# Optimization experiments

Hardware: AMD Instinct MI355X
Metric: run time of the kernel (lower is better)

Reference implementation:

```python
import jax, jax.numpy as jnp
import numpy as np

D_MODEL = 1024
DIM_FF = 4096
N_EXPERTS = 8
TOPK = 2
N_TOKENS = 8192


def setup_inputs() -> dict:
    key = jax.random.key(0)
    ks = jax.random.split(key, 8)
    s_in = 1.0 / np.sqrt(D_MODEL)
    s_ff = 1.0 / np.sqrt(DIM_FF)
    x = jax.random.normal(ks[0], (N_TOKENS, D_MODEL), dtype=jnp.float32)
    Wg = jax.random.uniform(ks[1], (D_MODEL, N_EXPERTS), minval=-s_in, maxval=s_in, dtype=jnp.float32)
    bg = jax.random.uniform(ks[2], (N_EXPERTS,), minval=-s_in, maxval=s_in, dtype=jnp.float32)
    W1 = jax.random.uniform(ks[3], (N_EXPERTS, D_MODEL, DIM_FF), minval=-s_in, maxval=s_in, dtype=jnp.float32)
    b1 = jax.random.uniform(ks[4], (N_EXPERTS, DIM_FF), minval=-s_in, maxval=s_in, dtype=jnp.float32)
    W2 = jax.random.uniform(ks[5], (N_EXPERTS, DIM_FF, D_MODEL), minval=-s_ff, maxval=s_ff, dtype=jnp.float32)
    b2 = jax.random.uniform(ks[6], (N_EXPERTS, D_MODEL), minval=-s_ff, maxval=s_ff, dtype=jnp.float32)
    return {"x": x, "Wg": Wg, "bg": bg, "W1": W1, "b1": b1, "W2": W2, "b2": b2}


def reference(x, Wg, bg, W1, b1, W2, b2):
    # Gate: softmax over experts
    w = jax.nn.softmax(x @ Wg + bg, axis=-1)  # [N, E]
    # Sparse gating: keep top-k, renormalize (matches torch scatter mask)
    _, idx = jax.lax.top_k(w, TOPK)  # [N, K]
    n = w.shape[0]
    mask = jnp.zeros_like(w).at[jnp.arange(n)[:, None], idx].set(1.0)
    w = w * mask
    w = w / (jnp.sum(w, axis=-1, keepdims=True) + 1e-9)
    # Dense per-expert FFN (exact GELU, as torch nn.GELU default)
    h = jax.nn.gelu(jnp.einsum('nd,edf->enf', x, W1) + b1[:, None, :], approximate=False)  # [E,N,F]
    y = jnp.einsum('enf,efd->end', h, W2) + b2[:, None, :]  # [E,N,D]
    out = jnp.einsum('ne,end->nd', w, y)  # weighted combine
    return out
```

## Files before the change

### kernel.cpp

```cpp
#include <hip/hip_runtime.h>
#include <cstdint>

typedef unsigned short u16;
typedef unsigned int u32;

#define N_TOKENS 8192
#define D_MODEL 1024
#define DIM_FF 4096
#define N_EXPERTS 8
#define MAX_SLOTS (N_TOKENS * 2)

typedef __bf16 bf16x8 __attribute__((ext_vector_type(8)));
typedef float f32x4 __attribute__((ext_vector_type(4)));

__device__ __forceinline__ u16 f2bf(float f) {
  u32 u = __float_as_uint(f);
  u32 r = (u + 0x7FFFu + ((u >> 16) & 1u)) >> 16;
  return (u16)r;
}
__device__ __forceinline__ u16 bfc(float f) {
  __bf16 b = (__bf16)f;
  return __builtin_bit_cast(u16, b);
}

__device__ __forceinline__ void gl2lds16(const void* g, void* l) {
  __builtin_amdgcn_global_load_lds(
      (__attribute__((address_space(1))) void*)(g),
      (__attribute__((address_space(3))) void*)(l), 16, 0, 0);
}

__global__ __launch_bounds__(256) void gate_kernel(
    const float* __restrict__ x, const float* __restrict__ Wg,
    const float* __restrict__ bg, int* __restrict__ eidx,
    float* __restrict__ ew, u16* __restrict__ xb) {
  int tok = (int)((blockIdx.x * 256 + threadIdx.x) >> 6);
  int lane = threadIdx.x & 63;
  const float* xr = x + (size_t)tok * D_MODEL;
  u16* xbr = xb + (size_t)tok * D_MODEL;
  float acc[8] = {0.f, 0.f, 0.f, 0.f, 0.f, 0.f, 0.f, 0.f};
#pragma unroll
  for (int j = 0; j < 8; ++j) {
    int d = 2 * lane + 128 * j;
    float2 xv = *(const float2*)(xr + d);
    float4 wa0 = *(const float4*)(Wg + d * 8);
    float4 wb0 = *(const float4*)(Wg + d * 8 + 4);
    float4 wa1 = *(const float4*)(Wg + d * 8 + 8);
    float4 wb1 = *(const float4*)(Wg + d * 8 + 12);
    acc[0] += xv.x * wa0.x + xv.y * wa1.x;
    acc[1] += xv.x * wa0.y + xv.y * wa1.y;
    acc[2] += xv.x * wa0.z + xv.y * wa1.z;
    acc[3] += xv.x * wa0.w + xv.y * wa1.w;
    acc[4] += xv.x * wb0.x + xv.y * wb1.x;
    acc[5] += xv.x * wb0.y + xv.y * wb1.y;
    acc[6] += xv.x * wb0.z + xv.y * wb1.z;
    acc[7] += xv.x * wb0.w + xv.y * wb1.w;
    u32 pk = (u32)f2bf(xv.x) | ((u32)f2bf(xv.y) << 16);
    *(u32*)(xbr + d) = pk;
  }
#pragma unroll
  for (int off = 32; off > 0; off >>= 1) {
#pragma unroll
    for (int e = 0; e < 8; ++e) acc[e] += __shfl_xor(acc[e], off, 64);
  }
  if (lane == 0) {
    float p[8], m = -1e30f;
#pragma unroll
    for (int e = 0; e < 8; ++e) { p[e] = acc[e] + bg[e]; m = fmaxf(m, p[e]); }
    float s = 0.f;
#pragma unroll
    for (int e = 0; e < 8; ++e) { p[e] = __expf(p[e] - m); s += p[e]; }
#pragma unroll
    for (int e = 0; e < 8; ++e) p[e] /= s;
    int i0 = 0;
#pragma unroll
    for (int e = 1; e < 8; ++e) if (p[e] > p[i0]) i0 = e;
    int i1 = (i0 == 0) ? 1 : 0;
#pragma unroll
    for (int e = 0; e < 8; ++e) if (e != i0 && p[e] > p[i1]) i1 = e;
    float denom = p[i0] + p[i1] + 1e-9f;
    eidx[2 * tok] = i0; eidx[2 * tok + 1] = i1;
    ew[2 * tok] = p[i0] / denom; ew[2 * tok + 1] = p[i1] / denom;
  }
}

__global__ __launch_bounds__(256) void count_kernel(const int* __restrict__ eidx,
                                                    int* __restrict__ counts) {
  __shared__ int lc[16];
  int tid = threadIdx.x;
  if (tid < 16) lc[tid] = 0;
  __syncthreads();
  int t = blockIdx.x * 256 + tid;
  atomicAdd(&lc[2 * eidx[2 * t]], 1);
  atomicAdd(&lc[2 * eidx[2 * t + 1] + 1], 1);
  __syncthreads();
  if (tid < 16) atomicAdd(&counts[tid], lc[tid]);
}

__global__ __launch_bounds__(256) void fill_kernel(
    const int* __restrict__ eidx, const float* __restrict__ ew,
    const int* __restrict__ counts, int* __restrict__ fill,
    int* __restrict__ rowtok, float* __restrict__ rowwt) {
  __shared__ int lc[16];
  __shared__ int lbase[16];
  __shared__ int loff[16];
  int tid = threadIdx.x;
  if (tid < 16) lc[tid] = 0;
  __syncthreads();
  int t = blockIdx.x * 256 + tid;
  int e0 = eidx[2 * t], e1 = eidx[2 * t + 1];
  int p0 = atomicAdd(&lc[2 * e0], 1);
  int p1 = atomicAdd(&lc[2 * e1 + 1], 1);
  __syncthreads();
  if (tid < 16) lbase[tid] = atomicAdd(&fill[tid], lc[tid]);
  if (tid == 64) {
    int o = 0;
    for (int g = 0; g < 16; ++g) { loff[g] = o; o += counts[g]; }
  }
  __syncthreads();
  int pos0 = loff[2 * e0] + lbase[2 * e0] + p0;
  int pos1 = loff[2 * e1 + 1] + lbase[2 * e1 + 1] + p1;
  rowtok[pos0] = t; rowwt[pos0] = ew[2 * t];
  rowtok[pos1] = t; rowwt[pos1] = ew[2 * t + 1];
}

__global__ __launch_bounds__(256) void transpose_cvt(const float* __restrict__ in,
                                                     u16* __restrict__ out, int R, int C) {
  int e = blockIdx.z;
  const float* ip = in + (size_t)e * R * C;
  u16* op = out + (size_t)e * R * C;
  int c0 = blockIdx.x * 64, r0 = blockIdx.y * 64;
  __shared__ __align__(16) u16 t[64 * 68];
  int tid = threadIdx.x;
  int c4 = (tid & 15) * 4;
#pragma unroll
  for (int p = 0; p < 4; ++p) {
    int r = (tid >> 4) + 16 * p;
    float4 v = *(const float4*)(ip + (size_t)(r0 + r) * C + c0 + c4);
    uint2 pk;
    pk.x = (u32)bfc(v.x) | ((u32)bfc(v.y) << 16);
    pk.y = (u32)bfc(v.z) | ((u32)bfc(v.w) << 16);
    *(uint2*)&t[r * 68 + c4] = pk;
  }
  __syncthreads();
  int pair = tid >> 3;
  int r8 = (tid & 7) * 8;
  int c = 2 * pair;
  u32 u[8];
#pragma unroll
  for (int j = 0; j < 8; ++j) u[j] = *(const u32*)&t[(r8 + j) * 68 + c];
  uint4 lo, hi;
  lo.x = (u[0] & 0xffffu) | (u[1] << 16);
  lo.y = (u[2] & 0xffffu) | (u[3] << 16);
  lo.z = (u[4] & 0xffffu) | (u[5] << 16);
  lo.w = (u[6] & 0xffffu) | (u[7] << 16);
  hi.x = (u[0] >> 16) | (u[1] & 0xffff0000u);
  hi.y = (u[2] >> 16) | (u[3] & 0xffff0000u);
  hi.z = (u[4] >> 16) | (u[5] & 0xffff0000u);
  hi.w = (u[6] >> 16) | (u[7] & 0xffff0000u);
  *(uint4*)(op + (size_t)(c0 + c) * R + r0 + r8) = lo;
  *(uint4*)(op + (size_t)(c0 + c + 1) * R + r0 + r8) = hi;
}

__global__ __launch_bounds__(256) void fc1_kernel(
    const u16* __restrict__ xb, const u16* __restrict__ w1t,
    const float* __restrict__ b1, const int* __restrict__ rowtok,
    const int* __restrict__ counts, u16* __restrict__ H) {
  const int b = blockIdx.x;
  const int e = b & 7;
  const int lin = b >> 3;
  const int rt = lin & 63;
  const int ct = lin >> 6;
  int base = 0;
#pragma unroll
  for (int g = 0; g < 16; ++g) base += (g < 2 * e) ? counts[g] : 0;
  const int count = counts[2 * e] + counts[2 * e + 1];
  if (rt * 128 >= count) return;

  __shared__ __align__(16) __bf16 As[128 * 32];
  __shared__ __align__(16) __bf16 Bs[128 * 32];

  const int tid = threadIdx.x;
  const int lane = tid & 63;
  const int wave = tid >> 6;

  const int ra = tid >> 2;
  const int lastslot = base + count - 1;
  int s0 = base + rt * 128 + ra;       if (s0 > lastslot) s0 = lastslot;
  int s1 = base + rt * 128 + ra + 64;  if (s1 > lastslot) s1 = lastslot;
  const size_t koff = (size_t)(tid & 3) * 8;
  const u16* ga0 = xb + (size_t)rowtok[s0] * D_MODEL + koff;
  const u16* ga1 = xb + (size_t)rowtok[s1] * D_MODEL + koff;
  const u16* gb0 = w1t + (size_t)e * DIM_FF * D_MODEL + (size_t)(ct * 128 + ra) * D_MODEL + koff;
  const u16* gb1 = gb0 + (size_t)64 * D_MODEL;

  __bf16* lA0 = As + tid * 8;
  __bf16* lA1 = As + (tid + 256) * 8;
  __bf16* lB0 = Bs + tid * 8;
  __bf16* lB1 = Bs + (tid + 256) * 8;

  const int wm = (wave & 1) * 64;
  const int wn = (wave >> 1) * 64;
  const int quad = lane >> 4;
  const int lc = lane & 15;
  const __bf16* Ap = As + (wm + lc) * 32 + quad * 8;
  const __bf16* Bp = Bs + (wn + lc) * 32 + quad * 8;

  f32x4 acc[4][4];
#pragma unroll
  for (int i = 0; i < 4; ++i)
#pragma unroll
    for (int j = 0; j < 4; ++j) acc[i][j] = (f32x4)0.0f;

  for (int kt = 0; kt < D_MODEL / 32; ++kt) {
    gl2lds16(ga0 + kt * 32, lA0);
    gl2lds16(ga1 + kt * 32, lA1);
    gl2lds16(gb0 + kt * 32, lB0);
    gl2lds16(gb1 + kt * 32, lB1);
    __syncthreads();
    bf16x8 af[4], bfr[4];
#pragma unroll
    for (int mi = 0; mi < 4; ++mi) af[mi] = *(const bf16x8*)(Ap + mi * 16 * 32);
#pragma unroll
    for (int ni = 0; ni < 4; ++ni) bfr[ni] = *(const bf16x8*)(Bp + ni * 16 * 32);
#pragma unroll
    for (int mi = 0; mi < 4; ++mi)
#pragma unroll
      for (int ni = 0; ni < 4; ++ni)
        acc[mi][ni] = __builtin_amdgcn_mfma_f32_16x16x32_bf16(af[mi], bfr[ni], acc[mi][ni], 0, 0, 0);
    __syncthreads();
  }

  float bias[4];
#pragma unroll
  for (int ni = 0; ni < 4; ++ni) bias[ni] = b1[e * DIM_FF + ct * 128 + wn + ni * 16 + lc];
#pragma unroll
  for (int mi = 0; mi < 4; ++mi) {
#pragma unroll
    for (int r = 0; r < 4; ++r) {
      int m = wm + mi * 16 + quad * 4 + r;
      int grow = rt * 128 + m;
      if (grow < count) {
        size_t rowbase = (size_t)(base + grow) * DIM_FF + ct * 128 + wn;
#pragma unroll
        for (int ni = 0; ni < 4; ++ni) {
          float v = acc[mi][ni][r] + bias[ni];
          float t3 = v * (1.0f + 0.044715f * v * v);
          float u = __builtin_amdgcn_exp2f(fminf(2.302208f * t3, 80.0f));
          float h = v * u * __builtin_amdgcn_rcpf(u + 1.0f);
          H[rowbase + ni * 16 + lc] = f2bf(h);
        }
      }
    }
  }
}

__global__ __launch_bounds__(256) void fc2_kernel(
    const u16* __restrict__ H, const u16* __restrict__ w2t,
    const float* __restrict__ b2, const int* __restrict__ rowtok,
    const float* __restrict__ rowwt, const int* __restrict__ counts,
    float* __restrict__ out) {
  const int b = blockIdx.x;
  const int e = b & 7;
  const int lin = b >> 3;
  const int rt = lin & 63;
  const int ct = (lin >> 6) & 7;
  const int ks = lin >> 9;
  int base = 0;
#pragma unroll
  for (int g = 0; g < 16; ++g) base += (g < 2 * e) ? counts[g] : 0;
  const int cnt = counts[2 * e] + counts[2 * e + 1];
  if (rt * 128 >= cnt) return;

  __shared__ __align__(16) __bf16 As[128 * 32];
  __shared__ __align__(16) __bf16 Bs[128 * 32];

  const int tid = threadIdx.x;
  const int lane = tid & 63;
  const int wave = tid >> 6;

  const int ra = tid >> 2;
  const size_t koff = (size_t)(tid & 3) * 8 + (size_t)ks * (DIM_FF / 2);
  const u16* ga0 = H + (size_t)(base + rt * 128 + ra) * DIM_FF + koff;
  const u16* ga1 = ga0 + (size_t)64 * DIM_FF;
  const u16* gb0 = w2t + (size_t)e * D_MODEL * DIM_FF + (size_t)(ct * 128 + ra) * DIM_FF + koff;
  const u16* gb1 = gb0 + (size_t)64 * DIM_FF;

  __bf16* lA0 = As + tid * 8;
  __bf16* lA1 = As + (tid + 256) * 8;
  __bf16* lB0 = Bs + tid * 8;
  __bf16* lB1 = Bs + (tid + 256) * 8;

  const int wm = (wave & 1) * 64;
  const int wn = (wave >> 1) * 64;
  const int quad = lane >> 4;
  const int lc = lane & 15;
  const __bf16* Ap = As + (wm + lc) * 32 + quad * 8;
  const __bf16* Bp = Bs + (wn + lc) * 32 + quad * 8;

  f32x4 acc[4][4];
#pragma unroll
  for (int i = 0; i < 4; ++i)
#pragma unroll
    for (int j = 0; j < 4; ++j) acc[i][j] = (f32x4)0.0f;

  for (int kt = 0; kt < DIM_FF / 32 / 2; ++kt) {
    gl2lds16(ga0 + kt * 32, lA0);
    gl2lds16(ga1 + kt * 32, lA1);
    gl2lds16(gb0 + kt * 32, lB0);
    gl2lds16(gb1 + kt * 32, lB1);
    __syncthreads();
    bf16x8 af[4], bfr[4];
#pragma unroll
    for (int mi = 0; mi < 4; ++mi) af[mi] = *(const bf16x8*)(Ap + mi * 16 * 32);
#pragma unroll
    for (int ni = 0; ni < 4; ++ni) bfr[ni] = *(const bf16x8*)(Bp + ni * 16 * 32);
#pragma unroll
    for (int mi = 0; mi < 4; ++mi)
#pragma unroll
      for (int ni = 0; ni < 4; ++ni)
        acc[mi][ni] = __builtin_amdgcn_mfma_f32_16x16x32_bf16(af[mi], bfr[ni], acc[mi][ni], 0, 0, 0);
    __syncthreads();
  }

  float bias[4];
#pragma unroll
  for (int ni = 0; ni < 4; ++ni)
    bias[ni] = (ks == 0) ? b2[e * D_MODEL + ct * 128 + wn + ni * 16 + lc] : 0.0f;

#pragma unroll
  for (int mi = 0; mi < 4; ++mi) {
#pragma unroll
    for (int r = 0; r < 4; ++r) {
      int m = wm + mi * 16 + quad * 4 + r;
      int grow = rt * 128 + m;
      if (grow < cnt) {
        int slot = base + grow;
        float wt = rowwt[slot];
        float* orow = out + (size_t)rowtok[slot] * D_MODEL + ct * 128 + wn;
#pragma unroll
        for (int ni = 0; ni < 4; ++ni)
          unsafeAtomicAdd(orow + ni * 16 + lc, wt * (acc[mi][ni][r] + bias[ni]));
      }
    }
  }
}

extern "C" void kernel_launch(void* const* d_in, const int* in_sizes, int n_in,
                              void* d_out, int out_size, void* d_ws, size_t ws_size,
                              hipStream_t stream) {
  (void)in_sizes; (void)n_in; (void)ws_size; (void)out_size;
  const float* x  = (const float*)d_in[0];
  const float* Wg = (const float*)d_in[1];
  const float* bg = (const float*)d_in[2];
  const float* W1 = (const float*)d_in[3];
  const float* b1 = (const float*)d_in[4];
  const float* W2 = (const float*)d_in[5];
  const float* b2 = (const float*)d_in[6];
  float* out = (float*)d_out;

  char* ws = (char*)d_ws;
  size_t off = 0;
  int*   counts  = (int*)(ws + 0);
  int*   fill    = (int*)(ws + 128);
  off = 4096;
  int*   eidx    = (int*)(ws + off); off += 65536;
  float* ew      = (float*)(ws + off); off += 65536;
  int*   rowtok  = (int*)(ws + off); off += 65536;
  float* rowwt   = (float*)(ws + off); off += 65536;
  u16*   xb      = (u16*)(ws + off); off += (size_t)N_TOKENS * D_MODEL * 2;
  u16*   w1t     = (u16*)(ws + off);
  u16*   w2t     = w1t;
  off += (size_t)N_EXPERTS * DIM_FF * D_MODEL * 2;
  u16*   H       = (u16*)(ws + off);
  off += (size_t)(MAX_SLOTS + 128) * DIM_FF * 2;

  hipMemsetAsync(ws, 0, 4096, stream);
  hipMemsetAsync(out, 0, (size_t)N_TOKENS * D_MODEL * sizeof(float), stream);

  gate_kernel<<<N_TOKENS / 4, 256, 0, stream>>>(x, Wg, bg, eidx, ew, xb);
  count_kernel<<<N_TOKENS / 256, 256, 0, stream>>>(eidx, counts);
  fill_kernel<<<N_TOKENS / 256, 256, 0, stream>>>(eidx, ew, counts, fill, rowtok, rowwt);
  transpose_cvt<<<dim3(DIM_FF / 64, D_MODEL / 64, N_EXPERTS), 256, 0, stream>>>(W1, w1t, D_MODEL, DIM_FF);
  fc1_kernel<<<N_EXPERTS * (DIM_FF / 128) * 64, 256, 0, stream>>>(xb, w1t, b1, rowtok, counts, H);
  transpose_cvt<<<dim3(D_MODEL / 64, DIM_FF / 64, N_EXPERTS), 256, 0, stream>>>(W2, w2t, DIM_FF, D_MODEL);
  fc2_kernel<<<N_EXPERTS * (D_MODEL / 128) * 64 * 2, 256, 0, stream>>>(H, w2t, b2, rowtok, rowwt, counts, out);
}
```

Measured before the change: 826.5 us.

## Rewrite expert GEMMs as 256x256 tiles with 8-wave double-buffered LDS pipeline

Measured after the change: 1.011 ms. 22.3% more time.

```diff
diff --git a/kernel.cpp b/kernel.cpp
--- a/kernel.cpp
+++ b/kernel.cpp
@@ -28,6 +28,20 @@
       (__attribute__((address_space(1))) void*)(g),
       (__attribute__((address_space(3))) void*)(l), 16, 0, 0);
 }
+
+__device__ __forceinline__ u32 lds_addr(const void* p) {
+  return (u32)(uintptr_t)(__attribute__((address_space(3))) const void*)p;
+}
+
+__device__ __forceinline__ bf16x8 dsr128(u32 addr) {
+  bf16x8 r;
+  asm volatile("ds_read_b128 %0, %1" : "=v"(r) : "v"(addr));
+  return r;
+}
+
+#define BARX() asm volatile("s_barrier" ::: "memory")
+#define LGKM0() do { asm volatile("s_waitcnt lgkmcnt(0)" ::: "memory"); __builtin_amdgcn_sched_barrier(0); } while (0)
+#define VMC(n) asm volatile("s_waitcnt vmcnt(" #n ")" ::: "memory")
 
 __global__ __launch_bounds__(256) void gate_kernel(
     const float* __restrict__ x, const float* __restrict__ Wg,
@@ -99,7 +113,8 @@
 __global__ __launch_bounds__(256) void fill_kernel(
     const int* __restrict__ eidx, const float* __restrict__ ew,
     const int* __restrict__ counts, int* __restrict__ fill,
-    int* __restrict__ rowtok, float* __restrict__ rowwt) {
+    int* __restrict__ rowtok, float* __restrict__ rowwt,
+    int* __restrict__ tmap) {
   __shared__ int lc[16];
   __shared__ int lbase[16];
   __shared__ int loff[16];
@@ -115,6 +130,15 @@
   if (tid == 64) {
     int o = 0;
     for (int g = 0; g < 16; ++g) { loff[g] = o; o += counts[g]; }
+  }
+  if (blockIdx.x == 0 && tid == 128) {
+    int nt2 = 0;
+    for (int ee = 0; ee < N_EXPERTS; ++ee) {
+      int c = counts[2 * ee] + counts[2 * ee + 1];
+      int ntile = (c + 255) >> 8;
+      for (int r = 0; r < ntile; ++r) tmap[1 + nt2++] = (ee << 16) | r;
+    }
+    tmap[0] = nt2;
   }
   __syncthreads();
   int pos0 = loff[2 * e0] + lbase[2 * e0] + p0;
@@ -161,86 +185,167 @@
   *(uint4*)(op + (size_t)(c0 + c + 1) * R + r0 + r8) = hi;
 }
 
-__global__ __launch_bounds__(256) void fc1_kernel(
+
+#define STG_A(buf, h, ktv) do { \
+  gl2lds16(aS##h##0 + (size_t)(ktv) * 64, lds + (buf) * 32768 + (h) * 16384 + 0 + tid * 16); \
+  gl2lds16(aS##h##1 + (size_t)(ktv) * 64, lds + (buf) * 32768 + (h) * 16384 + 8192 + tid * 16); \
+} while (0)
+#define STG_B(buf, h, ktv) do { \
+  gl2lds16(bS##h##0 + (size_t)(ktv) * 64, lds + 65536 + (buf) * 32768 + (h) * 16384 + 0 + tid * 16); \
+  gl2lds16(bS##h##1 + (size_t)(ktv) * 64, lds + 65536 + (buf) * 32768 + (h) * 16384 + 8192 + tid * 16); \
+} while (0)
+
+#define RDA(DST, BO, QO) do { \
+  _Pragma("unroll") \
+  for (int mi_ = 0; mi_ < 4; ++mi_) { \
+    DST[mi_][0] = dsr128(aR0 + (BO) + (QO) + mi_ * 2048); \
+    DST[mi_][1] = dsr128(aR1 + (BO) + (QO) + mi_ * 2048); \
+  } \
+} while (0)
+#define RDB(DST, BO, HO) do { \
+  _Pragma("unroll") \
+  for (int ni_ = 0; ni_ < 2; ++ni_) { \
+    DST[ni_][0] = dsr128(bR0 + (BO) + (HO) + ni_ * 2048); \
+    DST[ni_][1] = dsr128(bR1 + (BO) + (HO) + ni_ * 2048); \
+  } \
+} while (0)
+
+#define QMM(MO, NO, AF, BF) do { \
+  __builtin_amdgcn_s_setprio(1); \
+  _Pragma("unroll") \
+  for (int mi_ = 0; mi_ < 4; ++mi_) \
+    _Pragma("unroll") \
+    for (int ni_ = 0; ni_ < 2; ++ni_) \
+      _Pragma("unroll") \
+      for (int ks_ = 0; ks_ < 2; ++ks_) \
+        acc[(MO) + mi_][(NO) + ni_] = __builtin_amdgcn_mfma_f32_16x16x32_bf16( \
+            AF[mi_][ks_], BF[ni_][ks_], acc[(MO) + mi_][(NO) + ni_], 0, 0, 0); \
+  __builtin_amdgcn_s_setprio(0); \
+} while (0)
+
+#define KITER(KT, NL) do { \
+   \
+  RDA(af, 0, 0); RDB(bl, 0, 0); \
+  STG_A(1, 0, (KT) + 1); \
+  BARX(); LGKM0(); \
+  QMM(0, 0, af, bl); \
+  BARX(); \
+   \
+  RDB(bh, 0, 4096); \
+  STG_A(1, 1, (KT) + 1); \
+  BARX(); LGKM0(); \
+  QMM(0, 2, af, bh); \
+  BARX(); \
+   \
+  RDA(ah, 0, 8192); \
+  if (NL) STG_B(0, 0, (KT) + 2); \
+  BARX(); LGKM0(); \
+  QMM(4, 0, ah, bl); \
+  BARX(); \
+   \
+  if (NL) { STG_B(0, 1, (KT) + 2); VMC(4); } else { VMC(0); } \
+  BARX(); \
+  QMM(4, 2, ah, bh); \
+  BARX(); \
+   \
+  RDA(af, 32768, 0); RDB(bl, 32768, 0); \
+  if (NL) STG_A(0, 0, (KT) + 2); \
+  BARX(); LGKM0(); \
+  QMM(0, 0, af, bl); \
+  BARX(); \
+   \
+  RDB(bh, 32768, 4096); \
+  if (NL) STG_A(0, 1, (KT) + 2); \
+  BARX(); LGKM0(); \
+  QMM(0, 2, af, bh); \
+  BARX(); \
+   \
+  RDA(ah, 32768, 8192); \
+  if (NL) STG_B(1, 0, (KT) + 3); \
+  BARX(); LGKM0(); \
+  QMM(4, 0, ah, bl); \
+  BARX(); \
+   \
+  if (NL) { STG_B(1, 1, (KT) + 3); VMC(4); } \
+  BARX(); \
+  QMM(4, 2, ah, bh); \
+  BARX(); \
+} while (0)
+
+__global__ __launch_bounds__(512) void fc1_kernel(
     const u16* __restrict__ xb, const u16* __restrict__ w1t,
     const float* __restrict__ b1, const int* __restrict__ rowtok,
-    const int* __restrict__ counts, u16* __restrict__ H) {
-  const int b = blockIdx.x;
-  const int e = b & 7;
-  const int lin = b >> 3;
-  const int rt = lin & 63;
-  const int ct = lin >> 6;
+    const int* __restrict__ counts, const int* __restrict__ tmap,
+    u16* __restrict__ H) {
+  const int bx = blockIdx.x;
+  const int t = bx >> 4;
+  const int ct = bx & 15;
+  if (t >= tmap[0]) return;
+  const int ent = tmap[1 + t];
+  const int e = ent >> 16;
+  const int rt = ent & 0xffff;
   int base = 0;
 #pragma unroll
   for (int g = 0; g < 16; ++g) base += (g < 2 * e) ? counts[g] : 0;
   const int count = counts[2 * e] + counts[2 * e + 1];
-  if (rt * 128 >= count) return;
-
-  __shared__ __align__(16) __bf16 As[128 * 32];
-  __shared__ __align__(16) __bf16 Bs[128 * 32];
-
+
+  extern __shared__ char lds[];
   const int tid = threadIdx.x;
-  const int lane = tid & 63;
-  const int wave = tid >> 6;
-
-  const int ra = tid >> 2;
+
+  const int sub = tid >> 3;
+  const int csrc = (tid & 7) ^ (sub & 7);
   const int lastslot = base + count - 1;
-  int s0 = base + rt * 128 + ra;       if (s0 > lastslot) s0 = lastslot;
-  int s1 = base + rt * 128 + ra + 64;  if (s1 > lastslot) s1 = lastslot;
-  const size_t koff = (size_t)(tid & 3) * 8;
-  const u16* ga0 = xb + (size_t)rowtok[s0] * D_MODEL + koff;
-  const u16* ga1 = xb + (size_t)rowtok[s1] * D_MODEL + koff;
-  const u16* gb0 = w1t + (size_t)e * DIM_FF * D_MODEL + (size_t)(ct * 128 + ra) * D_MODEL + koff;
-  const u16* gb1 = gb0 + (size_t)64 * D_MODEL;
-
-  __bf16* lA0 = As + tid * 8;
-  __bf16* lA1 = As + (tid + 256) * 8;
-  __bf16* lB0 = Bs + tid * 8;
-  __bf16* lB1 = Bs + (tid + 256) * 8;
-
-  const int wm = (wave & 1) * 64;
-  const int wn = (wave >> 1) * 64;
-  const int quad = lane >> 4;
-  const int lc = lane & 15;
-  const __bf16* Ap = As + (wm + lc) * 32 + quad * 8;
-  const __bf16* Bp = Bs + (wn + lc) * 32 + quad * 8;
-
-  f32x4 acc[4][4];
-#pragma unroll
-  for (int i = 0; i < 4; ++i)
+  const u16* wb = w1t + (size_t)e * ((size_t)DIM_FF * D_MODEL);
+  int s00 = base + rt * 256 + 0 + sub;   if (s00 > lastslot) s00 = lastslot;
+  int s01 = base + rt * 256 + 64 + sub;  if (s01 > lastslot) s01 = lastslot;
+  int s10 = base + rt * 256 + 128 + sub; if (s10 > lastslot) s10 = lastslot;
+  int s11 = base + rt * 256 + 192 + sub; if (s11 > lastslot) s11 = lastslot;
+  const u16* aS00 = xb + (size_t)rowtok[s00] * D_MODEL + csrc * 8;
+  const u16* aS01 = xb + (size_t)rowtok[s01] * D_MODEL + csrc * 8;
+  const u16* aS10 = xb + (size_t)rowtok[s10] * D_MODEL + csrc * 8;
+  const u16* aS11 = xb + (size_t)rowtok[s11] * D_MODEL + csrc * 8;
+  const u16* bS00 = wb + (size_t)(ct * 256 + 0 + sub) * D_MODEL + csrc * 8;
+  const u16* bS01 = wb + (size_t)(ct * 256 + 64 + sub) * D_MODEL + csrc * 8;
+  const u16* bS10 = wb + (size_t)(ct * 256 + 128 + sub) * D_MODEL + csrc * 8;
+  const u16* bS11 = wb + (size_t)(ct * 256 + 192 + sub) * D_MODEL + csrc * 8;
+
+  const int lane = tid & 63, wid = tid >> 6;
+  const int wm = wid & 1, wn = wid >> 1;
+  const int lc = lane & 15, quad = lane >> 4;
+  const u32 lb = lds_addr(lds);
+  const u32 aR0 = lb + (u32)((wm * 128 + lc) * 128 + (((0 + quad) ^ (lc & 7)) * 16));
+  const u32 aR1 = lb + (u32)((wm * 128 + lc) * 128 + (((4 + quad) ^ (lc & 7)) * 16));
+  const u32 bR0 = lb + 65536u + (u32)((wn * 64 + lc) * 128 + (((0 + quad) ^ (lc & 7)) * 16));
+  const u32 bR1 = lb + 65536u + (u32)((wn * 64 + lc) * 128 + (((4 + quad) ^ (lc & 7)) * 16));
+
+  f32x4 acc[8][4];
+#pragma unroll
+  for (int i = 0; i < 8; ++i)
 #pragma unroll
     for (int j = 0; j < 4; ++j) acc[i][j] = (f32x4)0.0f;
-
-  for (int kt = 0; kt < D_MODEL / 32; ++kt) {
-    gl2lds16(ga0 + kt * 32, lA0);
-    gl2lds16(ga1 + kt * 32, lA1);
-    gl2lds16(gb0 + kt * 32, lB0);
-    gl2lds16(gb1 + kt * 32, lB1);
-    __syncthreads();
-    bf16x8 af[4], bfr[4];
-#pragma unroll
-    for (int mi = 0; mi < 4; ++mi) af[mi] = *(const bf16x8*)(Ap + mi * 16 * 32);
-#pragma unroll
-    for (int ni = 0; ni < 4; ++ni) bfr[ni] = *(const bf16x8*)(Bp + ni * 16 * 32);
-#pragma unroll
-    for (int mi = 0; mi < 4; ++mi)
-#pragma unroll
-      for (int ni = 0; ni < 4; ++ni)
-        acc[mi][ni] = __builtin_amdgcn_mfma_f32_16x16x32_bf16(af[mi], bfr[ni], acc[mi][ni], 0, 0, 0);
-    __syncthreads();
+  bf16x8 af[4][2], ah[4][2], bl[2][2], bh[2][2];
+
+  STG_B(0, 0, 0); STG_B(0, 1, 0); STG_A(0, 0, 0); STG_A(0, 1, 0);
+  STG_B(1, 0, 1); STG_B(1, 1, 1);
+  VMC(4); BARX();
+
+  const int NITER = (D_MODEL / 64) / 2;
+  for (int it = 0; it < NITER; ++it) {
+    const int kt = 2 * it;
+    const bool nl = (it < NITER - 1);
+    KITER(kt, nl);
   }
 
   float bias[4];
 #pragma unroll
-  for (int ni = 0; ni < 4; ++ni) bias[ni] = b1[e * DIM_FF + ct * 128 + wn + ni * 16 + lc];
-#pragma unroll
-  for (int mi = 0; mi < 4; ++mi) {
+  for (int ni = 0; ni < 4; ++ni) bias[ni] = b1[e * DIM_FF + ct * 256 + wn * 64 + ni * 16 + lc];
+#pragma unroll
+  for (int mi = 0; mi < 8; ++mi) {
 #pragma unroll
     for (int r = 0; r < 4; ++r) {
-      int m = wm + mi * 16 + quad * 4 + r;
-      int grow = rt * 128 + m;
+      int grow = rt * 256 + wm * 128 + mi * 16 + quad * 4 + r;
       if (grow < count) {
-        size_t rowbase = (size_t)(base + grow) * DIM_FF + ct * 128 + wn;
+        size_t rowbase = (size_t)(base + grow) * DIM_FF + ct * 256 + wn * 64;
 #pragma unroll
         for (int ni = 0; ni < 4; ++ni) {
           float v = acc[mi][ni][r] + bias[ni];
@@ -254,89 +359,81 @@
   }
 }
 
-__global__ __launch_bounds__(256) void fc2_kernel(
+__global__ __launch_bounds__(512) void fc2_kernel(
     const u16* __restrict__ H, const u16* __restrict__ w2t,
     const float* __restrict__ b2, const int* __restrict__ rowtok,
     const float* __restrict__ rowwt, const int* __restrict__ counts,
-    float* __restrict__ out) {
-  const int b = blockIdx.x;
-  const int e = b & 7;
-  const int lin = b >> 3;
-  const int rt = lin & 63;
-  const int ct = (lin >> 6) & 7;
-  const int ks = lin >> 9;
+    const int* __restrict__ tmap, float* __restrict__ out) {
+  const int bx = blockIdx.x;
+  const int t = bx >> 3;
+  const int c8 = bx & 7;
+  const int ct = c8 >> 1;
+  const int ks = c8 & 1;
+  if (t >= tmap[0]) return;
+  const int ent = tmap[1 + t];
+  const int e = ent >> 16;
+  const int rt = ent & 0xffff;
   int base = 0;
 #pragma unroll
   for (int g = 0; g < 16; ++g) base += (g < 2 * e) ? counts[g] : 0;
-  const int cnt = counts[2 * e] + counts[2 * e + 1];
-  if (rt * 128 >= cnt) return;
-
-  __shared__ __align__(16) __bf16 As[128 * 32];
-  __shared__ __align__(16) __bf16 Bs[128 * 32];
-
+  const int count = counts[2 * e] + counts[2 * e + 1];
+
+  extern __shared__ char lds[];
   const int tid = threadIdx.x;
-  const int lane = tid & 63;
-  const int wave = tid >> 6;
-
-  const int ra = tid >> 2;
-  const size_t koff = (size_t)(tid & 3) * 8 + (size_t)ks * (DIM_FF / 2);
-  const u16* ga0 = H + (size_t)(base + rt * 128 + ra) * DIM_FF + koff;
-  const u16* ga1 = ga0 + (size_t)64 * DIM_FF;
-  const u16* gb0 = w2t + (size_t)e * D_MODEL * DIM_FF + (size_t)(ct * 128 + ra) * DIM_FF + koff;
-  const u16* gb1 = gb0 + (size_t)64 * DIM_FF;
-
-  __bf16* lA0 = As + tid * 8;
-  __bf16* lA1 = As + (tid + 256) * 8;
-  __bf16* lB0 = Bs + tid * 8;
-  __bf16* lB1 = Bs + (tid + 256) * 8;
-
-  const int wm = (wave & 1) * 64;
-  const int wn = (wave >> 1) * 64;
-  const int quad = lane >> 4;
-  const int lc = lane & 15;
-  const __bf16* Ap = As + (wm + lc) * 32 + quad * 8;
-  const __bf16* Bp = Bs + (wn + lc) * 32 + quad * 8;
-
-  f32x4 acc[4][4];
-#pragma unroll
-  for (int i = 0; i < 4; ++i)
+
+  const int sub = tid >> 3;
+  const int csrc = (tid & 7) ^ (sub & 7);
+  const u16* hb = H + (size_t)(base + rt * 256) * DIM_FF + (size_t)ks * (DIM_FF / 2) + csrc * 8;
+  const u16* aS00 = hb + (size_t)(0 + sub) * DIM_FF;
+  const u16* aS01 = hb + (size_t)(64 + sub) * DIM_FF;
+  const u16* aS10 = hb + (size_t)(128 + sub) * DIM_FF;
+  const u16* aS11 = hb + (size_t)(192 + sub) * DIM_FF;
+  const u16* wb = w2t + (size_t)e * ((size_t)D_MODEL * DIM_FF) + (size_t)ks * (DIM_FF / 2) + csrc * 8;
+  const u16* bS00 = wb + (size_t)(ct * 256 + 0 + sub) * DIM_FF;
+  const u16* bS01 = wb + (size_t)(ct * 256 + 64 + sub) * DIM_FF;
+  const u16* bS10 = wb + (size_t)(ct * 256 + 128 + sub) * DIM_FF;
+  const u16* bS11 = wb + (size_t)(ct * 256 + 192 + sub) * DIM_FF;
+
+  const int lane = tid & 63, wid = tid >> 6;
+  const int wm = wid & 1, wn = wid >> 1;
+  const int lc = lane & 15, quad = lane >> 4;
+  const u32 lb = lds_addr(lds);
+  const u32 aR0 = lb + (u32)((wm * 128 + lc) * 128 + (((0 + quad) ^ (lc & 7)) * 16));
+  const u32 aR1 = lb + (u32)((wm * 128 + lc) * 128 + (((4 + quad) ^ (lc & 7)) * 16));
+  const u32 bR0 = lb + 65536u + (u32)((wn * 64 + lc) * 128 + (((0 + quad) ^ (lc & 7)) * 16));
+  const u32 bR1 = lb + 65536u + (u32)((wn * 64 + lc) * 128 + (((4 + quad) ^ (lc & 7)) * 16));
+
+  f32x4 acc[8][4];
+#pragma unroll
+  for (int i = 0; i < 8; ++i)
 #pragma unroll
     for (int j = 0; j < 4; ++j) acc[i][j] = (f32x4)0.0f;
-
-  for (int kt = 0; kt < DIM_FF / 32 / 2; ++kt) {
-    gl2lds16(ga0 + kt * 32, lA0);
-    gl2lds16(ga1 + kt * 32, lA1);
-    gl2lds16(gb0 + kt * 32, lB0);
-    gl2lds16(gb1 + kt * 32, lB1);
-    __syncthreads();
-    bf16x8 af[4], bfr[4];
-#pragma unroll
-    for (int mi = 0; mi < 4; ++mi) af[mi] = *(const bf16x8*)(Ap + mi * 16 * 32);
-#pragma unroll
-    for (int ni = 0; ni < 4; ++ni) bfr[ni] = *(const bf16x8*)(Bp + ni * 16 * 32);
-#pragma unroll
-    for (int mi = 0; mi < 4; ++mi)
-#pragma unroll
-      for (int ni = 0; ni < 4; ++ni)
-        acc[mi][ni] = __builtin_amdgcn_mfma_f32_16x16x32_bf16(af[mi], bfr[ni], acc[mi][ni], 0, 0, 0);
-    __syncthreads();
+  bf16x8 af[4][2], ah[4][2], bl[2][2], bh[2][2];
+
+  STG_B(0, 0, 0); STG_B(0, 1, 0); STG_A(0, 0, 0); STG_A(0, 1, 0);
+  STG_B(1, 0, 1); STG_B(1, 1, 1);
+  VMC(4); BARX();
+
+  const int NITER = ((DIM_FF / 2) / 64) / 2;
+  for (int it = 0; it < NITER; ++it) {
+    const int kt = 2 * it;
+    const bool nl = (it < NITER - 1);
+    KITER(kt, nl);
   }
 
   float bias[4];
 #pragma unroll
   for (int ni = 0; ni < 4; ++ni)
-    bias[ni] = (ks == 0) ? b2[e * D_MODEL + ct * 128 + wn + ni * 16 + lc] : 0.0f;
-
-#pragma unroll
-  for (int mi = 0; mi < 4; ++mi) {
+    bias[ni] = (ks == 0) ? b2[e * D_MODEL + ct * 256 + wn * 64 + ni * 16 + lc] : 0.0f;
+#pragma unroll
+  for (int mi = 0; mi < 8; ++mi) {
 #pragma unroll
     for (int r = 0; r < 4; ++r) {
-      int m = wm + mi * 16 + quad * 4 + r;
-      int grow = rt * 128 + m;
-      if (grow < cnt) {
+      int grow = rt * 256 + wm * 128 + mi * 16 + quad * 4 + r;
+      if (grow < count) {
         int slot = base + grow;
         float wt = rowwt[slot];
-        float* orow = out + (size_t)rowtok[slot] * D_MODEL + ct * 128 + wn;
+        float* orow = out + (size_t)rowtok[slot] * D_MODEL + ct * 256 + wn * 64;
 #pragma unroll
         for (int ni = 0; ni < 4; ++ni)
           unsafeAtomicAdd(orow + ni * 16 + lc, wt * (acc[mi][ni][r] + bias[ni]));
@@ -362,6 +459,7 @@
   size_t off = 0;
   int*   counts  = (int*)(ws + 0);
   int*   fill    = (int*)(ws + 128);
+  int*   tmap    = (int*)(ws + 256);
   off = 4096;
   int*   eidx    = (int*)(ws + off); off += 65536;
   float* ew      = (float*)(ws + off); off += 65536;
@@ -372,16 +470,23 @@
   u16*   w2t     = w1t;
   off += (size_t)N_EXPERTS * DIM_FF * D_MODEL * 2;
   u16*   H       = (u16*)(ws + off);
-  off += (size_t)(MAX_SLOTS + 128) * DIM_FF * 2;
+  off += (size_t)(MAX_SLOTS + 256) * DIM_FF * 2;
+
+  static int attr_done = 0;
+  if (!attr_done) {
+    hipFuncSetAttribute((const void*)fc1_kernel, hipFuncAttributeMaxDynamicSharedMemorySize, 131072);
+    hipFuncSetAttribute((const void*)fc2_kernel, hipFuncAttributeMaxDynamicSharedMemorySize, 131072);
+    attr_done = 1;
+  }
 
   hipMemsetAsync(ws, 0, 4096, stream);
   hipMemsetAsync(out, 0, (size_t)N_TOKENS * D_MODEL * sizeof(float), stream);
 
   gate_kernel<<<N_TOKENS / 4, 256, 0, stream>>>(x, Wg, bg, eidx, ew, xb);
   count_kernel<<<N_TOKENS / 256, 256, 0, stream>>>(eidx, counts);
-  fill_kernel<<<N_TOKENS / 256, 256, 0, stream>>>(eidx, ew, counts, fill, rowtok, rowwt);
+  fill_kernel<<<N_TOKENS / 256, 256, 0, stream>>>(eidx, ew, counts, fill, rowtok, rowwt, tmap);
   transpose_cvt<<<dim3(DIM_FF / 64, D_MODEL / 64, N_EXPERTS), 256, 0, stream>>>(W1, w1t, D_MODEL, DIM_FF);
-  fc1_kernel<<<N_EXPERTS * (DIM_FF / 128) * 64, 256, 0, stream>>>(xb, w1t, b1, rowtok, counts, H);
+  fc1_kernel<<<72 * 16, 512, 131072, stream>>>(xb, w1t, b1, rowtok, counts, tmap, H);
   transpose_cvt<<<dim3(D_MODEL / 64, DIM_FF / 64, N_EXPERTS), 256, 0, stream>>>(W2, w2t, DIM_FF, D_MODEL);
-  fc2_kernel<<<N_EXPERTS * (D_MODEL / 128) * 64 * 2, 256, 0, stream>>>(H, w2t, b2, rowtok, rowwt, counts, out);
-}
+  fc2_kernel<<<72 * 8, 512, 131072, stream>>>(H, w2t, b2, rowtok, rowwt, counts, tmap, out);
+}
```
